# Performance work log

Hardware: AMD Instinct MI355X
Metric: run time of the kernel (lower is better)

The kernel has to match this reference:

```python
import jax, jax.numpy as jnp
import numpy as np

B, L, C, H, V = 64, 512, 256, 4, 32000
D = C // H
DIL = (1, 2, 4)
WIN = 3
NC = (50, 20)
NEG = -1e9


def setup_inputs() -> dict:
    key = jax.random.key(0)
    ks = jax.random.split(key, 20)
    g = lambda i, shape: jax.random.normal(ks[i], shape, jnp.float32) * 0.05
    Lay = len(DIL)
    x = jax.random.randint(ks[0], (B, L), 0, V)
    emb = g(1, (V, C)).at[0].set(0.0)  # padding_idx=0 row is zero
    return dict(
        x=x, emb=emb, pos=g(2, (L, C)),
        gp_W=g(3, (Lay, C, C)), gp_as=g(4, (Lay, H, D)), gp_ad=g(5, (Lay, H, D)),
        gf_W=g(6, (Lay, C, C)), gf_as=g(7, (Lay, H, D)), gf_ad=g(8, (Lay, H, D)),
        msg_W=g(9, (Lay, C, 2 * C)), msg_b=jnp.zeros((Lay, C), jnp.float32),
        gru_Wih=g(10, (Lay, 3 * C, C)), gru_bih=jnp.zeros((Lay, 3 * C), jnp.float32),
        gru_Whh=g(11, (Lay, 3 * C, C)), gru_bhh=jnp.zeros((Lay, 3 * C), jnp.float32),
        ln_g=jnp.ones((Lay, C), jnp.float32), ln_b=jnp.zeros((Lay, C), jnp.float32),
        pool_w=g(12, (C,)), pool_b=jnp.zeros((), jnp.float32),
        h0_W=g(13, (NC[0], C)), h0_b=jnp.zeros((NC[0],), jnp.float32),
        h1_W=g(14, (NC[1], C)), h1_b=jnp.zeros((NC[1],), jnp.float32),
    )


def _dense_gat(x, W, a_src, a_dst, adj):
    # x: [B,L,C], W: [C_out,C_in], a_*: [H,D], adj: [B,L,L] bool
    b, l, _ = x.shape
    h = jnp.einsum('blc,oc->blo', x, W).reshape(b, l, H, D).transpose(0, 2, 1, 3)  # [B,H,L,D]
    s = jnp.einsum('bhld,hd->bhl', h, a_src)
    d = jnp.einsum('bhld,hd->bhl', h, a_dst)
    e = s[:, :, :, None] + d[:, :, None, :]            # [B,H,L,L]
    e = jnp.where(e > 0, e, 0.2 * e)                   # LeakyReLU(0.2)
    e = jnp.where(adj[:, None, :, :], e, NEG)
    alpha = jax.nn.softmax(e, axis=-1)                 # dropout is identity in eval
    out = jnp.einsum('bhij,bhjd->bhid', alpha, h)
    return out.transpose(0, 2, 1, 3).reshape(b, l, C)


def _forward(x, emb, pos, gp_W, gp_as, gp_ad, gf_W, gf_as, gf_ad,
             msg_W, msg_b, gru_Wih, gru_bih, gru_Whh, gru_bhh,
             ln_g, ln_b, pool_w, pool_b, h0_W, h0_b, h1_W, h1_b):
    mask = x != 0                                      # [B,L]
    mf = mask.astype(jnp.float32)[..., None]           # [B,L,1]
    h = (emb[x] + pos[None, :, :] * mf) * mf
    logical = jnp.clip(jnp.cumsum(mask.astype(jnp.int32), axis=1) - 1, 0)
    valid = mask[:, None, :] & mask[:, :, None]        # [B,L,L]
    eye = jnp.eye(L, dtype=bool)[None]
    for l in range(len(DIL)):
        dil = DIL[l]
        diff = logical[:, :, None] - logical[:, None, :]
        ad = jnp.abs(diff)
        in_win = (ad <= WIN * dil) & (ad % dil == 0)
        adj_p = (valid & in_win & (diff < 0)) | eye
        adj_f = (valid & in_win & (diff > 0)) | eye
        m_p = _dense_gat(h, gp_W[l], gp_as[l], gp_ad[l], adj_p)
        m_f = _dense_gat(h, gf_W[l], gf_as[l], gf_ad[l], adj_f)
        m = jnp.concatenate([m_p, m_f], axis=-1)
        m = jax.nn.relu(jnp.einsum('blk,ck->blc', m, msg_W[l]) + msg_b[l])
        # GRUCell(input=m, hidden=h), PyTorch gate order: r,z,n
        gi = jnp.einsum('blc,gc->blg', m, gru_Wih[l]) + gru_bih[l]
        gh = jnp.einsum('blc,gc->blg', h, gru_Whh[l]) + gru_bhh[l]
        ir, iz, inn = jnp.split(gi, 3, axis=-1)
        hr, hz, hn = jnp.split(gh, 3, axis=-1)
        r = jax.nn.sigmoid(ir + hr)
        z = jax.nn.sigmoid(iz + hz)
        n = jnp.tanh(inn + r * hn)
        h_new = (1.0 - z) * n + z * h
        mu = jnp.mean(h_new, axis=-1, keepdims=True)
        var = jnp.mean(jnp.square(h_new - mu), axis=-1, keepdims=True)
        h_new = (h_new - mu) * jax.lax.rsqrt(var + 1e-5) * ln_g[l] + ln_b[l]
        h = h_new * mf
    # attention pooling over sequence (masked softmax on linear scores)
    sc = jnp.einsum('blc,c->bl', h, pool_w) + pool_b
    sc = jnp.where(mask, sc, NEG)
    a = jax.nn.softmax(sc, axis=-1)
    pooled = jnp.einsum('bl,blc->bc', a, h)            # dropout identity in eval
    o0 = pooled @ h0_W.T + h0_b
    o1 = pooled @ h1_W.T + h1_b
    return jnp.concatenate([o0, o1], axis=-1)          # [B, 50+20]


def reference(x, emb, pos, gp_W, gp_as, gp_ad, gf_W, gf_as, gf_ad,
              msg_W, msg_b, gru_Wih, gru_bih, gru_Whh, gru_bhh,
              ln_g, ln_b, pool_w, pool_b, h0_W, h0_b, h1_W, h1_b):
    return _forward(x, emb, pos, gp_W, gp_as, gp_ad, gf_W, gf_as, gf_ad,
                    msg_W, msg_b, gru_Wih, gru_bih, gru_Whh, gru_bhh,
                    ln_g, ln_b, pool_w, pool_b, h0_W, h0_b, h1_W, h1_b)
```

## Files before the change

kernel.cpp:

```cpp
#include <hip/hip_runtime.h>
#include <math.h>

#define B_ 64
#define L_ 512
#define C_ 256
#define H_ 4
#define LAY 3
#define NEGV -1e9f

typedef __attribute__((ext_vector_type(8))) short short8;
typedef __attribute__((ext_vector_type(4))) short short4v;
typedef __attribute__((ext_vector_type(4))) float floatx4;

static __device__ __forceinline__ float rcp_(float x) { return __builtin_amdgcn_rcpf(x); }
static __device__ __forceinline__ float sig_(float x) { return rcp_(1.f + __expf(-x)); }
static __device__ __forceinline__ float tanh_(float x) {
    float e = __expf(2.f * x);
    return 1.f - 2.f * rcp_(e + 1.f);
}

static __device__ __forceinline__ short f2bf(float f) {
    unsigned x = __float_as_uint(f);
    x += 0x7fffu + ((x >> 16) & 1u);
    return (short)(x >> 16);
}
static __device__ __forceinline__ float bf2f(short s) {
    return __uint_as_float(((unsigned)(unsigned short)s) << 16);
}

static __device__ __forceinline__ int tok_swizzle(int blk) {
    int c8 = blk & 7, i = blk >> 3;
    return (c8 + 8 * (i >> 5)) * 128 + (i & 31) * 4;
}

static __device__ __forceinline__ void gl_lds16(const short* g, short* l) {
    __builtin_amdgcn_global_load_lds(
        (const __attribute__((address_space(1))) unsigned int*)g,
        (__attribute__((address_space(3))) unsigned int*)l, 16, 0, 0);
}

#define CF() asm volatile("" ::: "memory")

#define PR_N0 (3 * 640 * 256)
#define PR_N1 (3 * 256 * 512)
#define PR_N2 (3 * 1024 * 512)
#define PR_N3 (3 * 1024)
#define PR_N4 (B_ * 70)
#define PR_TOT (PR_N0 + PR_N1 + PR_N2 + PR_N3 + PR_N4)

__global__ void prep_all(const float* __restrict__ gpW, const float* __restrict__ gfW,
                         const float* __restrict__ gpas, const float* __restrict__ gpad,
                         const float* __restrict__ gfas, const float* __restrict__ gfad,
                         const float* __restrict__ msgW,
                         const float* __restrict__ Wih, const float* __restrict__ Whh,
                         const float* __restrict__ bih, const float* __restrict__ bhh,
                         short* __restrict__ Wc, short* __restrict__ msgWb,
                         short* __restrict__ Bc, float* __restrict__ bias4,
                         float* __restrict__ outz) {
    int i = blockIdx.x * 256 + threadIdx.x;
    if (i < PR_N0) {
        int k = i & 255;
        int r = (i >> 8) % 640;
        int l = i / (640 * 256);
        float v = 0.f;
        if (r < 256) {
            v = gpW[((size_t)l * 256 + r) * 256 + k];
        } else if (r < 512) {
            v = gfW[((size_t)l * 256 + (r - 256)) * 256 + k];
        } else {
            int n = r - 512;
            if (n < 16) {
                int type = n >> 3, dir = (n >> 2) & 1, hh = n & 3;
                const float* a = type ? (dir ? gfad : gpad) : (dir ? gfas : gpas);
                const float* W = dir ? gfW : gpW;
                for (int j = 0; j < 64; j++) {
                    float av = a[l * 256 + hh * 64 + j];
                    float wv = W[((size_t)l * 256 + hh * 64 + j) * 256 + k];
                    v = fmaf(av, wv, v);
                }
            }
        }
        Wc[i] = f2bf(v);
        return;
    }
    i -= PR_N0;
    if (i < PR_N1) { msgWb[i] = f2bf(msgW[i]); return; }
    i -= PR_N1;
    if (i < PR_N2) {
        int k = i & 511, np = (i >> 9) & 1023, l = i >> 19;
        int ch = np >> 2, g = np & 3;
        float v = 0.f;
        if (g < 2) {
            v = (k < 256) ? Wih[((size_t)l * 768 + g * 256 + ch) * 256 + k]
                          : Whh[((size_t)l * 768 + g * 256 + ch) * 256 + (k - 256)];
        } else if (g == 2) {
            if (k < 256) v = Wih[((size_t)l * 768 + 512 + ch) * 256 + k];
        } else {
            if (k >= 256) v = Whh[((size_t)l * 768 + 512 + ch) * 256 + (k - 256)];
        }
        Bc[i] = f2bf(v);
        return;
    }
    i -= PR_N2;
    if (i < PR_N3) {
        int np = i & 1023, l = i >> 10;
        int ch = np >> 2, g = np & 3;
        float v;
        if (g < 2)       v = bih[l * 768 + g * 256 + ch] + bhh[l * 768 + g * 256 + ch];
        else if (g == 2) v = bih[l * 768 + 512 + ch];
        else             v = bhh[l * 768 + 512 + ch];
        bias4[i] = v;
        return;
    }
    i -= PR_N3;
    if (i < PR_N4) outz[i] = 0.f;
}

__global__ __launch_bounds__(512) void scan_embed(
    const int* __restrict__ x, const float* __restrict__ emb,
    const float* __restrict__ pos, short* __restrict__ hb,
    int* __restrict__ mask, int* __restrict__ logical,
    int* __restrict__ pol, int* __restrict__ nvalid) {
    if (blockIdx.x < 64) {
        int b = blockIdx.x, t = threadIdx.x;
        __shared__ int s[L_];
        int m = (x[b * L_ + t] != 0) ? 1 : 0;
        s[t] = m;
        __syncthreads();
        for (int off = 1; off < L_; off <<= 1) {
            int v = (t >= off) ? s[t - off] : 0;
            __syncthreads();
            s[t] += v;
            __syncthreads();
        }
        int cum = s[t];
        int lg = cum - 1; if (lg < 0) lg = 0;
        mask[b * L_ + t] = m;
        logical[b * L_ + t] = lg;
        if (m) pol[b * L_ + lg] = t;
        if (t == L_ - 1) nvalid[b] = cum;
    } else {
        int t = threadIdx.x & 255, sub = threadIdx.x >> 8;
        int blk2 = (blockIdx.x - 64) * 2 + sub;
        int bl = tok_swizzle(blk2) + (t >> 6);
        int lane = t & 63;
        int xv = x[bl];
        float mf = (xv != 0) ? 1.f : 0.f;
        int l = bl & (L_ - 1);
        float4 e = *(const float4*)&emb[(size_t)xv * C_ + lane * 4];
        float4 p = *(const float4*)&pos[(size_t)l * C_ + lane * 4];
        short4v hv4;
        hv4.x = f2bf((e.x + p.x * mf) * mf);
        hv4.y = f2bf((e.y + p.y * mf) * mf);
        hv4.z = f2bf((e.z + p.z * mf) * mf);
        hv4.w = f2bf((e.w + p.w * mf) * mf);
        *(short4v*)&hb[(size_t)bl * C_ + lane * 4] = hv4;
    }
}

static __device__ __forceinline__ short8 lds_rd8(const short* p) {
    return *(const short8*)p;
}

template <int MH>
static __device__ __forceinline__ void ld_af(const short* bufA, int wm, int q, int t16,
                                             short8 af[4][2]) {
#pragma unroll
    for (int mfl = 0; mfl < 4; ++mfl) {
        int row = wm * 128 + (MH * 4 + mfl) * 16 + t16;
#pragma unroll
        for (int ks = 0; ks < 2; ++ks) {
            int cg = (ks * 4 + q) ^ (row & 7);
            af[mfl][ks] = lds_rd8(&bufA[row * 64 + cg * 8]);
        }
    }
}

template <int NH>
static __device__ __forceinline__ void ld_bf(const short* bufB, int wn, int q, int t16,
                                             short8 bf[2][2]) {
#pragma unroll
    for (int nfl = 0; nfl < 2; ++nfl) {
        int row = wn * 64 + (NH * 2 + nfl) * 16 + t16;
#pragma unroll
        for (int ks = 0; ks < 2; ++ks) {
            int cg = (ks * 4 + q) ^ (row & 7);
            bf[nfl][ks] = lds_rd8(&bufB[row * 64 + cg * 8]);
        }
    }
}

static __device__ __forceinline__ void ld_bf32(const short* bufB, int wn, int q, int t16,
                                               short8 bf[2][2]) {
#pragma unroll
    for (int nfl = 0; nfl < 2; ++nfl) {
        int row = wn * 32 + nfl * 16 + t16;
#pragma unroll
        for (int ks = 0; ks < 2; ++ks) {
            int cg = (ks * 4 + q) ^ (row & 7);
            bf[nfl][ks] = lds_rd8(&bufB[row * 64 + cg * 8]);
        }
    }
}

template <int MH, int NH>
static __device__ __forceinline__ void mfma_q(const short8 af[4][2], const short8 bf[2][2],
                                              floatx4 acc[4][8]) {
    __builtin_amdgcn_s_setprio(1);
#pragma unroll
    for (int ks = 0; ks < 2; ++ks)
#pragma unroll
        for (int mfl = 0; mfl < 4; ++mfl)
#pragma unroll
            for (int nfl = 0; nfl < 2; ++nfl)
                acc[NH * 2 + nfl][MH * 4 + mfl] = __builtin_amdgcn_mfma_f32_16x16x32_bf16(
                    bf[nfl][ks], af[mfl][ks], acc[NH * 2 + nfl][MH * 4 + mfl], 0, 0, 0);
    __builtin_amdgcn_s_setprio(0);
}

template <int MH>
static __device__ __forceinline__ void mfma_m(const short8 af[4][2], const short8 bf[2][2],
                                              floatx4 acc[2][8]) {
    __builtin_amdgcn_s_setprio(1);
#pragma unroll
    for (int ks = 0; ks < 2; ++ks)
#pragma unroll
        for (int mfl = 0; mfl < 4; ++mfl)
#pragma unroll
            for (int nfl = 0; nfl < 2; ++nfl)
                acc[nfl][MH * 4 + mfl] = __builtin_amdgcn_mfma_f32_16x16x32_bf16(
                    bf[nfl][ks], af[mfl][ks], acc[nfl][MH * 4 + mfl], 0, 0, 0);
    __builtin_amdgcn_s_setprio(0);
}

__global__ __launch_bounds__(512, 2) void projssd_deep(const short* __restrict__ A0,
                                                       const short* __restrict__ Bw,
                                                       short* __restrict__ hpb2,
                                                       float* __restrict__ Ssd) {
    __shared__ short lds[2][24576];
    const int id = blockIdx.x;
    const int j = id >> 3;
    const int cb = j >> 4;
    const int rb = (id & 7) * 16 + (j & 15);
    const int tid = threadIdx.x;
    const int wave = tid >> 6, lane = tid & 63;
    const int wm = wave >> 2, wn = wave & 3;
    const int q = lane >> 4, t16 = lane & 15;
    const size_t arow0 = (size_t)rb * 256;
    const short* Bb = Bw + (size_t)cb * 128 * 256;

    floatx4 acc[2][8];
#pragma unroll
    for (int i = 0; i < 2; i++)
#pragma unroll
        for (int jj = 0; jj < 8; jj++) acc[i][jj] = (floatx4)0.f;

    auto stageA = [&](int t, int Hh) {
        short* bufA = lds[t & 1];
#pragma unroll
        for (int u = 0; u < 2; ++u) {
            int unit = u * 512 + tid;
            int row = Hh * 128 + (unit >> 3);
            int cs = (unit & 7) ^ (row & 7);
            gl_lds16(A0 + (arow0 + (size_t)row) * 256 + t * 64 + cs * 8,
                     bufA + Hh * 8192 + unit * 8);
        }
    };
    auto stageB = [&](int t) {
        short* bufB = lds[t & 1] + 16384;
#pragma unroll
        for (int u = 0; u < 2; ++u) {
            int unit = u * 512 + tid;
            int row = unit >> 3;
            int cs = (unit & 7) ^ (row & 7);
            gl_lds16(Bb + (size_t)row * 256 + t * 64 + cs * 8, bufB + unit * 8);
        }
    };

    stageA(0, 0); stageA(0, 1); stageB(0); stageB(1);
    asm volatile("s_waitcnt vmcnt(2)" ::: "memory");
    CF(); __builtin_amdgcn_s_barrier(); CF();

    short8 af[4][2], bfr[2][2];

#pragma unroll
    for (int t = 0; t < 4; ++t) {
        const short* bufA = lds[t & 1];
        const short* bufB = lds[t & 1] + 16384;

        ld_af<0>(bufA, wm, q, t16, af);
        ld_bf32(bufB, wn, q, t16, bfr);
        if (t < 3) { stageA(t + 1, 0); stageA(t + 1, 1); }
        CF(); __builtin_amdgcn_s_barrier();
        asm volatile("s_waitcnt lgkmcnt(0)" ::: "memory");
        __builtin_amdgcn_sched_barrier(0);
        mfma_m<0>(af, bfr, acc);
        CF(); __builtin_amdgcn_s_barrier(); CF();

        ld_af<1>(bufA, wm, q, t16, af);
        if (t < 2) stageB(t + 2);
        CF(); __builtin_amdgcn_s_barrier();
        asm volatile("s_waitcnt lgkmcnt(0)" ::: "memory");
        __builtin_amdgcn_sched_barrier(0);
        mfma_m<1>(af, bfr, acc);
        if (t < 2)       asm volatile("s_waitcnt vmcnt(2)" ::: "memory");
        else if (t == 2) asm volatile("s_waitcnt vmcnt(0)" ::: "memory");
        CF(); __builtin_amdgcn_s_barrier(); CF();
    }

    if (cb < 4) {
        short* sO = (short*)lds;
#pragma unroll
        for (int nf = 0; nf < 2; nf++) {
            int chl = wn * 32 + nf * 16 + q * 4;
#pragma unroll
            for (int mf = 0; mf < 8; mf++) {
                int rowl = wm * 128 + mf * 16 + t16;
                short4v pk;
                pk.x = f2bf(acc[nf][mf][0]);
                pk.y = f2bf(acc[nf][mf][1]);
                pk.z = f2bf(acc[nf][mf][2]);
                pk.w = f2bf(acc[nf][mf][3]);
                *(short4v*)&sO[rowl * 132 + chl] = pk;
            }
        }
        __syncthreads();
#pragma unroll
        for (int it = 0; it < 8; ++it) {
            int unit = it * 512 + tid;
            int rowl = unit >> 4, ck = unit & 15;
            *(short8*)&hpb2[(arow0 + rowl) * 512 + cb * 128 + ck * 8] =
                *(const short8*)&sO[rowl * 132 + ck * 8];
        }
    } else {
        if (wn == 0) {
            int chl = q * 4;
            if (chl < 16) {
#pragma unroll
                for (int mf = 0; mf < 8; mf++) {
                    int rowl = wm * 128 + mf * 16 + t16;
                    float4 pk = make_float4(acc[0][mf][0], acc[0][mf][1],
                                            acc[0][mf][2], acc[0][mf][3]);
                    *(float4*)&Ssd[(arow0 + rowl) * 16 + chl] = pk;
                }
            }
        }
    }
}

__global__ __launch_bounds__(512, 2) void gru_bgemm(const short* __restrict__ mmb,
                                                    const short* __restrict__ hb_in,
                                                    const short* __restrict__ Bw,
                                                    short* __restrict__ hn2b,
                                                    const float* __restrict__ bias4) {
    __shared__ short lds[2][32768];
    const int id = blockIdx.x;
    const int rb = 16 * (id & 7) + (id >> 5);
    const int cb = (id >> 3) & 3;
    const int tid = threadIdx.x;
    const int wave = tid >> 6, lane = tid & 63;
    const int wm = wave >> 2, wn = wave & 3;
    const int q = lane >> 4, t16 = lane & 15;
    const size_t arow0 = (size_t)rb * 256;
    const short* Bb = Bw + (size_t)cb * 256 * 512;
    const int ord0 = (5 + cb) & 7;

    floatx4 acc[4][8];
#pragma unroll
    for (int i = 0; i < 4; i++)
#pragma unroll
        for (int jj = 0; jj < 8; jj++) acc[i][jj] = (floatx4)0.f;

    auto stageA = [&](int i, int Hh) {
        int tt = (ord0 + i) & 7;
        const short* Asrc = (tt < 4) ? (mmb + tt * 64) : (hb_in + (tt - 4) * 64);
        short* bufA = lds[i & 1];
#pragma unroll
        for (int u = 0; u < 2; ++u) {
            int unit = u * 512 + tid;
            int row = Hh * 128 + (unit >> 3);
            int cs = (unit & 7) ^ (row & 7);
            gl_lds16(Asrc + (arow0 + (size_t)row) * 256 + cs * 8,
                     bufA + Hh * 8192 + unit * 8);
        }
    };
    auto stageB = [&](int i, int Hh) {
        int tt = (ord0 + i) & 7;
        short* bufB = lds[i & 1] + 16384;
#pragma unroll
        for (int u = 0; u < 2; ++u) {
            int unit = u * 512 + tid;
            int row = Hh * 128 + (unit >> 3);
            int cs = (unit & 7) ^ (row & 7);
            gl_lds16(Bb + (size_t)row * 512 + tt * 64 + cs * 8,
                     bufB + Hh * 8192 + unit * 8);
        }
    };

    stageA(0, 0); stageA(0, 1); stageB(0, 0); stageB(0, 1);
    stageA(1, 0); stageA(1, 1); stageB(1, 0); stageB(1, 1);
    asm volatile("s_waitcnt vmcnt(8)" ::: "memory");
    CF(); __builtin_amdgcn_s_barrier(); CF();

    short8 af[4][2], b0[2][2], b1[2][2];

#pragma unroll
    for (int t = 0; t < 8; ++t) {
        const short* bufA = lds[t & 1];
        const short* bufB = lds[t & 1] + 16384;

        ld_af<0>(bufA, wm, q, t16, af);
        ld_bf<0>(bufB, wn, q, t16, b0);
        CF(); __builtin_amdgcn_s_barrier();
        asm volatile("s_waitcnt lgkmcnt(0)" ::: "memory");
        __builtin_amdgcn_sched_barrier(0);
        mfma_q<0, 0>(af, b0, acc);
        CF(); __builtin_amdgcn_s_barrier(); CF();

        ld_bf<1>(bufB, wn, q, t16, b1);
        CF(); __builtin_amdgcn_s_barrier();
        asm volatile("s_waitcnt lgkmcnt(0)" ::: "memory");
        __builtin_amdgcn_sched_barrier(0);
        mfma_q<0, 1>(af, b1, acc);
        CF(); __builtin_amdgcn_s_barrier(); CF();

        ld_af<1>(bufA, wm, q, t16, af);
        if (t < 6) { stageB(t + 2, 0); stageB(t + 2, 1); }
        CF(); __builtin_amdgcn_s_barrier();
        asm volatile("s_waitcnt lgkmcnt(0)" ::: "memory");
        __builtin_amdgcn_sched_barrier(0);
        mfma_q<1, 1>(af, b1, acc);
        CF(); __builtin_amdgcn_s_barrier(); CF();

        if (t < 6) { stageA(t + 2, 0); stageA(t + 2, 1); }
        CF(); __builtin_amdgcn_s_barrier();
        mfma_q<1, 0>(af, b0, acc);
        if (t < 6)       asm volatile("s_waitcnt vmcnt(8)" ::: "memory");
        else if (t == 6) asm volatile("s_waitcnt vmcnt(0)" ::: "memory");
        CF(); __builtin_amdgcn_s_barrier(); CF();
    }

    const short* hpt = lds[1];
    short* sO = (short*)lds;
#pragma unroll
    for (int nf = 0; nf < 4; nf++) {
        int chl = wn * 16 + nf * 4 + q;
        int col0 = cb * 256 + wn * 64 + nf * 16 + q * 4;
        float4 bv4 = *(const float4*)&bias4[col0];
#pragma unroll
        for (int mf = 0; mf < 8; mf++) {
            int rowl = wm * 128 + mf * 16 + t16;
            float hp = bf2f(hpt[rowl * 64 + (((chl >> 3) ^ (rowl & 7)) << 3) + (chl & 7)]);
            float r = sig_(acc[nf][mf][0] + bv4.x);
            float z = sig_(acc[nf][mf][1] + bv4.y);
            float nv = tanh_((acc[nf][mf][2] + bv4.z) + r * (acc[nf][mf][3] + bv4.w));
            sO[rowl * 72 + chl] = f2bf((1.f - z) * nv + z * hp);
        }
    }
    __syncthreads();
#pragma unroll
    for (int it = 0; it < 4; ++it) {
        int unit = it * 512 + tid;
        int rowl = unit >> 3, ck = unit & 7;
        *(short8*)&hn2b[(arow0 + rowl) * 256 + cb * 64 + ck * 8] =
            *(const short8*)&sO[rowl * 72 + ck * 8];
    }
}

__global__ __launch_bounds__(512, 2) void msg_bgemm(const short* __restrict__ A0,
                                                    const short* __restrict__ Bw,
                                                    short* __restrict__ Cout,
                                                    const float* __restrict__ bias) {
    __shared__ short lds[2][24576];
    const int id = blockIdx.x;
    const int j = id >> 3;
    const int rb = (id & 7) * 16 + (j & 15);
    const int cb = j >> 4;
    const int tid = threadIdx.x;
    const int wave = tid >> 6, lane = tid & 63;
    const int wm = wave >> 2, wn = wave & 3;
    const int q = lane >> 4, t16 = lane & 15;
    const size_t arow0 = (size_t)rb * 256;
    const short* Bb = Bw + (size_t)cb * 128 * 512;

    floatx4 acc[2][8];
#pragma unroll
    for (int i = 0; i < 2; i++)
#pragma unroll
        for (int jj = 0; jj < 8; jj++) acc[i][jj] = (floatx4)0.f;

    auto stageA = [&](int t, int Hh) {
        short* bufA = lds[t & 1];
#pragma unroll
        for (int u = 0; u < 2; ++u) {
            int unit = u * 512 + tid;
            int row = Hh * 128 + (unit >> 3);
            int cs = (unit & 7) ^ (row & 7);
            gl_lds16(A0 + (arow0 + (size_t)row) * 512 + t * 64 + cs * 8,
                     bufA + Hh * 8192 + unit * 8);
        }
    };
    auto stageB = [&](int t) {
        short* bufB = lds[t & 1] + 16384;
#pragma unroll
        for (int u = 0; u < 2; ++u) {
            int unit = u * 512 + tid;
            int row = unit >> 3;
            int cs = (unit & 7) ^ (row & 7);
            gl_lds16(Bb + (size_t)row * 512 + t * 64 + cs * 8, bufB + unit * 8);
        }
    };

    stageA(0, 0); stageA(0, 1); stageB(0); stageB(1);
    asm volatile("s_waitcnt vmcnt(2)" ::: "memory");
    CF(); __builtin_amdgcn_s_barrier(); CF();

    short8 af[4][2], bfr[2][2];

#pragma unroll 2
    for (int t = 0; t < 8; ++t) {
        const short* bufA = lds[t & 1];
        const short* bufB = lds[t & 1] + 16384;

        ld_af<0>(bufA, wm, q, t16, af);
        ld_bf32(bufB, wn, q, t16, bfr);
        if (t < 7) { stageA(t + 1, 0); stageA(t + 1, 1); }
        CF(); __builtin_amdgcn_s_barrier();
        asm volatile("s_waitcnt lgkmcnt(0)" ::: "memory");
        mfma_m<0>(af, bfr, acc);
        CF(); __builtin_amdgcn_s_barrier(); CF();

        ld_af<1>(bufA, wm, q, t16, af);
        if (t < 6) stageB(t + 2);
        CF(); __builtin_amdgcn_s_barrier();
        asm volatile("s_waitcnt lgkmcnt(0)" ::: "memory");
        mfma_m<1>(af, bfr, acc);
        if (t < 6)       asm volatile("s_waitcnt vmcnt(2)" ::: "memory");
        else if (t == 6) asm volatile("s_waitcnt vmcnt(0)" ::: "memory");
        CF(); __builtin_amdgcn_s_barrier(); CF();
    }

    short* sO = (short*)lds;
#pragma unroll
    for (int nf = 0; nf < 2; nf++) {
        int chl = wn * 32 + nf * 16 + q * 4;
        int col0 = cb * 128 + chl;
        float4 bv4 = *(const float4*)&bias[col0];
#pragma unroll
        for (int mf = 0; mf < 8; mf++) {
            int rowl = wm * 128 + mf * 16 + t16;
            short4v pk;
            pk.x = f2bf(fmaxf(acc[nf][mf][0] + bv4.x, 0.f));
            pk.y = f2bf(fmaxf(acc[nf][mf][1] + bv4.y, 0.f));
            pk.z = f2bf(fmaxf(acc[nf][mf][2] + bv4.z, 0.f));
            pk.w = f2bf(fmaxf(acc[nf][mf][3] + bv4.w, 0.f));
            *(short4v*)&sO[rowl * 132 + chl] = pk;
        }
    }
    __syncthreads();
#pragma unroll
    for (int it = 0; it < 8; ++it) {
        int unit = it * 512 + tid;
        int rowl = unit >> 4, ck = unit & 15;
        *(short8*)&Cout[(arow0 + rowl) * 256 + cb * 128 + ck * 8] =
            *(const short8*)&sO[rowl * 132 + ck * 8];
    }
}

__global__ __launch_bounds__(256) void ln_kernel(
    const short* __restrict__ hn2b, short* __restrict__ hb,
    const int* __restrict__ mask,
    const float* __restrict__ lng, const float* __restrict__ lnb) {
    int t = threadIdx.x;
    int bl = tok_swizzle(blockIdx.x) + (t >> 6);
    int lane = t & 63;
    short4v v4 = *(const short4v*)&hn2b[(size_t)bl * C_ + lane * 4];
    float v[4] = {bf2f(v4.x), bf2f(v4.y), bf2f(v4.z), bf2f(v4.w)};
    float s = (v[0] + v[1]) + (v[2] + v[3]);
    float ss = (v[0] * v[0] + v[1] * v[1]) + (v[2] * v[2] + v[3] * v[3]);
#pragma unroll
    for (int off = 32; off; off >>= 1) {
        s += __shfl_xor(s, off);
        ss += __shfl_xor(ss, off);
    }
    float mu = s * (1.f / 256.f);
    float var = ss * (1.f / 256.f) - mu * mu;
    float rstd = rsqrtf(fmaxf(var, 0.f) + 1e-5f);
    float4 lg = *(const float4*)&lng[lane * 4];
    float4 lb = *(const float4*)&lnb[lane * 4];
    float mfv = mask[bl] ? 1.f : 0.f;
    short4v yb;
    yb.x = f2bf(((v[0] - mu) * rstd * lg.x + lb.x) * mfv);
    yb.y = f2bf(((v[1] - mu) * rstd * lg.y + lb.y) * mfv);
    yb.z = f2bf(((v[2] - mu) * rstd * lg.z + lb.z) * mfv);
    yb.w = f2bf(((v[3] - mu) * rstd * lg.w + lb.w) * mfv);
    *(short4v*)&hb[(size_t)bl * C_ + lane * 4] = yb;
}

__global__ __launch_bounds__(256) void agg_fused(
    const short* __restrict__ hpb2, const float* __restrict__ S,
    const int* __restrict__ mask, const int* __restrict__ logical,
    const int* __restrict__ pol, const int* __restrict__ nvalid,
    short* __restrict__ m, int dil) {
    int t = threadIdx.x;
    int bl = tok_swizzle(blockIdx.x) + (t >> 6);
    int sub = t & 63;
    int dir = sub >> 5;
    int slot = sub & 31;
    int cb = slot * 8;
    int head = slot >> 3;
    int b = bl >> 9;

    int mi = mask[bl];
    int li = logical[bl];
    int nv = nvalid[b];
    int js[3]; int nn = 0;
    if (mi) {
#pragma unroll
        for (int k = 1; k <= 3; k++) {
            int lj = dir ? (li - k * dil) : (li + k * dil);
            if (lj >= 0 && lj < nv) js[nn++] = pol[b * L_ + lj];
        }
    }
    int sn = dir * 4 + head, dn = 8 + sn;
    float si = S[(size_t)bl * 16 + sn];
    float di = S[(size_t)bl * 16 + dn];
    float e0 = si + di; e0 = e0 > 0.f ? e0 : 0.2f * e0;
    float emax = e0, ev[3];
    for (int k = 0; k < nn; k++) {
        float djv = S[((size_t)(b * L_ + js[k])) * 16 + dn];
        float e = si + djv; e = e > 0.f ? e : 0.2f * e;
        ev[k] = e; emax = fmaxf(emax, e);
    }
    float w0 = __expf(e0 - emax), den = w0;
    float wv[3];
    for (int k = 0; k < nn; k++) { wv[k] = __expf(ev[k] - emax); den += wv[k]; }
    float rden = rcp_(den);

    size_t base = (size_t)bl * 512 + dir * 256 + cb;
    short8 vself = *(const short8*)&hpb2[base];
    float o[8];
#pragma unroll
    for (int j = 0; j < 8; j++) o[j] = w0 * bf2f(vself[j]);
    for (int k = 0; k < nn; k++) {
        short8 vn = *(const short8*)&hpb2[((size_t)(b * L_ + js[k])) * 512 + dir * 256 + cb];
#pragma unroll
        for (int j = 0; j < 8; j++) o[j] = fmaf(wv[k], bf2f(vn[j]), o[j]);
    }
    short8 ov;
#pragma unroll
    for (int j = 0; j < 8; j++) ov[j] = f2bf(o[j] * rden);
    *(short8*)&m[base] = ov;
}

__global__ __launch_bounds__(1024) void pool_head2(
    const short* __restrict__ hb, const int* __restrict__ mask,
    const float* __restrict__ pw, const float* __restrict__ pb,
    const float* __restrict__ h0W, const float* __restrict__ h0b,
    const float* __restrict__ h1W, const float* __restrict__ h1b,
    float* __restrict__ out) {
    int b = blockIdx.x >> 2, s = blockIdx.x & 3;
    int t = threadIdx.x;
    int lane = t & 63, wave = t >> 6;
    __shared__ float sc[L_];
    __shared__ float red[20];
    __shared__ float part[16][64];
    __shared__ float pooled[64];

    float4 wv = *(const float4*)&pw[lane * 4];
    for (int l = wave; l < L_; l += 16) {
        short4v hv = *(const short4v*)&hb[((size_t)b * L_ + l) * C_ + lane * 4];
        float p = bf2f(hv.x) * wv.x + bf2f(hv.y) * wv.y
                + bf2f(hv.z) * wv.z + bf2f(hv.w) * wv.w;
#pragma unroll
        for (int off = 32; off; off >>= 1) p += __shfl_down(p, off);
        if (lane == 0) sc[l] = mask[b * L_ + l] ? (p + pb[0]) : NEGV;
    }
    __syncthreads();

    float v = (t < L_) ? sc[t] : NEGV;
    float mx = v;
#pragma unroll
    for (int off = 32; off; off >>= 1) mx = fmaxf(mx, __shfl_down(mx, off));
    if (lane == 0) red[wave] = mx;
    __syncthreads();
    if (t == 0) {
        float g = red[0];
        for (int i = 1; i < 16; i++) g = fmaxf(g, red[i]);
        red[16] = g;
    }
    __syncthreads();
    float gmax = red[16];
    float e = (t < L_) ? __expf(v - gmax) : 0.f;
    float ssum = e;
#pragma unroll
    for (int off = 32; off; off >>= 1) ssum += __shfl_down(ssum, off);
    if (lane == 0) red[wave] = ssum;
    __syncthreads();
    if (t == 0) {
        float g = 0.f;
        for (int i = 0; i < 16; i++) g += red[i];
        red[17] = 1.f / g;
    }
    __syncthreads();
    if (t < L_) sc[t] = e * red[17];
    __syncthreads();

    {
        int c0 = t & 63, lw = t >> 6;
        const short* hcol = &hb[((size_t)b * L_ + lw * 32) * C_ + s * 64 + c0];
        const float* scg = &sc[lw * 32];
        float a0 = 0.f, a1 = 0.f;
        for (int l = 0; l < 32; l += 2) {
            a0 = fmaf(scg[l + 0], bf2f(hcol[(size_t)(l + 0) * C_]), a0);
            a1 = fmaf(scg[l + 1], bf2f(hcol[(size_t)(l + 1) * C_]), a1);
        }
        part[lw][c0] = a0 + a1;
    }
    __syncthreads();
    if (t < 64) {
        float p = 0.f;
        for (int i = 0; i < 16; i++) p += part[i][t];
        pooled[t] = p;
    }
    __syncthreads();

    for (int o = wave; o < 70; o += 16) {
        const float* W = (o < 50) ? (h0W + (size_t)o * C_) : (h1W + (size_t)(o - 50) * C_);
        float sv = pooled[lane] * W[s * 64 + lane];
#pragma unroll
        for (int off = 32; off; off >>= 1) sv += __shfl_down(sv, off);
        if (lane == 0) {
            float add = sv + ((s == 0) ? ((o < 50) ? h0b[o] : h1b[o - 50]) : 0.f);
            atomicAdd(&out[b * 70 + o], add);
        }
    }
}

extern "C" void kernel_launch(void* const* d_in, const int* in_sizes, int n_in,
                              void* d_out, int out_size, void* d_ws, size_t ws_size,
                              hipStream_t stream) {
    const int*   x    = (const int*)d_in[0];
    const float* emb  = (const float*)d_in[1];
    const float* pos  = (const float*)d_in[2];
    const float* gpW  = (const float*)d_in[3];
    const float* gpas = (const float*)d_in[4];
    const float* gpad = (const float*)d_in[5];
    const float* gfW  = (const float*)d_in[6];
    const float* gfas = (const float*)d_in[7];
    const float* gfad = (const float*)d_in[8];
    const float* msgW = (const float*)d_in[9];
    const float* msgb = (const float*)d_in[10];
    const float* Wih  = (const float*)d_in[11];
    const float* bih  = (const float*)d_in[12];
    const float* Whh  = (const float*)d_in[13];
    const float* bhh  = (const float*)d_in[14];
    const float* lng  = (const float*)d_in[15];
    const float* lnb  = (const float*)d_in[16];
    const float* pw   = (const float*)d_in[17];
    const float* pb   = (const float*)d_in[18];
    const float* h0W  = (const float*)d_in[19];
    const float* h0b  = (const float*)d_in[20];
    const float* h1W  = (const float*)d_in[21];
    const float* h1b  = (const float*)d_in[22];
    float* out = (float*)d_out;

    const size_t MW = 1024 * 1024;
    float* ws = (float*)d_ws;
    short* hn2b = (short*)ws;
    short* hb   = (short*)(ws + 8 * MW);
    short* mmb  = (short*)(ws + 12 * MW);
    float* Ssd  = ws + 12 * MW;
    short* hpb2 = (short*)(ws + 16 * MW);
    short* mb   = (short*)(ws + 24 * MW);
    short* Wcomb = (short*)(ws + 32 * MW);
    short* msgWb = Wcomb + 3 * 640 * 256;
    short* Bcat  = msgWb + 3 * 256 * 512;
    float* bias4 = (float*)(Bcat + 3 * 1024 * 512);
    int* mask    = (int*)(bias4 + 3 * 1024);
    int* logical = mask + B_ * L_;
    int* pol     = logical + B_ * L_;
    int* nvalid  = pol + B_ * L_;

    prep_all<<<(PR_TOT + 255) / 256, 256, 0, stream>>>(
        gpW, gfW, gpas, gpad, gfas, gfad, msgW, Wih, Whh, bih, bhh,
        Wcomb, msgWb, Bcat, bias4, out);

    scan_embed<<<64 + 4096, 512, 0, stream>>>(x, emb, pos, hb, mask, logical, pol, nvalid);

    const int DILS[LAY] = {1, 2, 4};

    for (int l = 0; l < LAY; l++) {
        int dil = DILS[l];
        projssd_deep<<<640, 512, 0, stream>>>(hb, Wcomb + (size_t)l * 640 * 256,
                                              hpb2, Ssd);
        agg_fused<<<8192, 256, 0, stream>>>(hpb2, Ssd, mask, logical, pol, nvalid, mb, dil);
        msg_bgemm<<<256, 512, 0, stream>>>(mb, msgWb + (size_t)l * 256 * 512,
                                           mmb, msgb + l * C_);
        gru_bgemm<<<512, 512, 0, stream>>>(mmb, hb, Bcat + (size_t)l * 1024 * 512,
                                           hn2b, bias4 + l * 1024);
        ln_kernel<<<8192, 256, 0, stream>>>(hn2b, hb, mask, lng + l * C_, lnb + l * C_);
    }

    pool_head2<<<B_ * 4, 1024, 0, stream>>>(hb, mask, pw, pb, h0W, h0b, h1W, h1b, out);
}
```

Measured before the change: 483.4 us.

## Restructure GRU GEMM to 32-wide K tiles with triple-buffered A

The GRU batched GEMM now walks K in 16 steps of 32 instead of 8 steps of 64. A uses a three-slot LDS ring and B a two-slot ring, which shrinks LDS from 128 KB to 80 KB. Launch bounds are raised to allow four blocks per SM, aiming for more occupancy and finer-grained load/compute overlap. The trade-off is twice as many barriers and waitcnt stalls per K, and a more intricate buffer mapping for reading the previous hidden state in the epilogue.

```diff
diff --git a/kernel.cpp b/kernel.cpp
--- a/kernel.cpp
+++ b/kernel.cpp
@@ -176,46 +176,17 @@
     }
 }
 
-template <int NH>
-static __device__ __forceinline__ void ld_bf(const short* bufB, int wn, int q, int t16,
-                                             short8 bf[2][2]) {
+static __device__ __forceinline__ void ld_bf32(const short* bufB, int wn, int q, int t16,
+                                               short8 bf[2][2]) {
 #pragma unroll
     for (int nfl = 0; nfl < 2; ++nfl) {
-        int row = wn * 64 + (NH * 2 + nfl) * 16 + t16;
+        int row = wn * 32 + nfl * 16 + t16;
 #pragma unroll
         for (int ks = 0; ks < 2; ++ks) {
             int cg = (ks * 4 + q) ^ (row & 7);
             bf[nfl][ks] = lds_rd8(&bufB[row * 64 + cg * 8]);
         }
     }
-}
-
-static __device__ __forceinline__ void ld_bf32(const short* bufB, int wn, int q, int t16,
-                                               short8 bf[2][2]) {
-#pragma unroll
-    for (int nfl = 0; nfl < 2; ++nfl) {
-        int row = wn * 32 + nfl * 16 + t16;
-#pragma unroll
-        for (int ks = 0; ks < 2; ++ks) {
-            int cg = (ks * 4 + q) ^ (row & 7);
-            bf[nfl][ks] = lds_rd8(&bufB[row * 64 + cg * 8]);
-        }
-    }
-}
-
-template <int MH, int NH>
-static __device__ __forceinline__ void mfma_q(const short8 af[4][2], const short8 bf[2][2],
-                                              floatx4 acc[4][8]) {
-    __builtin_amdgcn_s_setprio(1);
-#pragma unroll
-    for (int ks = 0; ks < 2; ++ks)
-#pragma unroll
-        for (int mfl = 0; mfl < 4; ++mfl)
-#pragma unroll
-            for (int nfl = 0; nfl < 2; ++nfl)
-                acc[NH * 2 + nfl][MH * 4 + mfl] = __builtin_amdgcn_mfma_f32_16x16x32_bf16(
-                    bf[nfl][ks], af[mfl][ks], acc[NH * 2 + nfl][MH * 4 + mfl], 0, 0, 0);
-    __builtin_amdgcn_s_setprio(0);
 }
 
 template <int MH>
@@ -230,6 +201,40 @@
             for (int nfl = 0; nfl < 2; ++nfl)
                 acc[nfl][MH * 4 + mfl] = __builtin_amdgcn_mfma_f32_16x16x32_bf16(
                     bf[nfl][ks], af[mfl][ks], acc[nfl][MH * 4 + mfl], 0, 0, 0);
+    __builtin_amdgcn_s_setprio(0);
+}
+
+template <int MH>
+static __device__ __forceinline__ void ld_af32(const short* bufA, int wm, int q, int t16,
+                                               short8 af[4]) {
+#pragma unroll
+    for (int mfl = 0; mfl < 4; ++mfl) {
+        int row = wm * 128 + (MH * 4 + mfl) * 16 + t16;
+        int cg = q ^ (row & 3);
+        af[mfl] = lds_rd8(&bufA[row * 32 + cg * 8]);
+    }
+}
+
+static __device__ __forceinline__ void ld_bfq(const short* bufB, int wn, int q, int t16,
+                                              short8 bf[4]) {
+#pragma unroll
+    for (int nf = 0; nf < 4; ++nf) {
+        int row = wn * 64 + nf * 16 + t16;
+        int cg = q ^ (row & 3);
+        bf[nf] = lds_rd8(&bufB[row * 32 + cg * 8]);
+    }
+}
+
+template <int MH>
+static __device__ __forceinline__ void mfma_h(const short8 af[4], const short8 bf[4],
+                                              floatx4 acc[4][8]) {
+    __builtin_amdgcn_s_setprio(1);
+#pragma unroll
+    for (int mfl = 0; mfl < 4; ++mfl)
+#pragma unroll
+        for (int nf = 0; nf < 4; ++nf)
+            acc[nf][MH * 4 + mfl] = __builtin_amdgcn_mfma_f32_16x16x32_bf16(
+                bf[nf], af[mfl], acc[nf][MH * 4 + mfl], 0, 0, 0);
     __builtin_amdgcn_s_setprio(0);
 }
 
@@ -348,12 +353,13 @@
     }
 }
 
-__global__ __launch_bounds__(512, 2) void gru_bgemm(const short* __restrict__ mmb,
+#define GA_OFF(k3) ((k3) == 0 ? 0 : ((k3) == 1 ? 16384 : 8192))
+__global__ __launch_bounds__(512, 4) void gru_bgemm(const short* __restrict__ mmb,
                                                     const short* __restrict__ hb_in,
                                                     const short* __restrict__ Bw,
                                                     short* __restrict__ hn2b,
                                                     const float* __restrict__ bias4) {
-    __shared__ short lds[2][32768];
+    __shared__ short lds[40960];
     const int id = blockIdx.x;
     const int rb = 16 * (id & 7) + (id >> 5);
     const int cb = (id >> 3) & 3;
@@ -363,7 +369,7 @@
     const int q = lane >> 4, t16 = lane & 15;
     const size_t arow0 = (size_t)rb * 256;
     const short* Bb = Bw + (size_t)cb * 256 * 512;
-    const int ord0 = (5 + cb) & 7;
+    const int ord0 = (2 * cb + 10) & 15;
 
     floatx4 acc[4][8];
 #pragma unroll
@@ -371,86 +377,75 @@
 #pragma unroll
         for (int jj = 0; jj < 8; jj++) acc[i][jj] = (floatx4)0.f;
 
-    auto stageA = [&](int i, int Hh) {
-        int tt = (ord0 + i) & 7;
-        const short* Asrc = (tt < 4) ? (mmb + tt * 64) : (hb_in + (tt - 4) * 64);
-        short* bufA = lds[i & 1];
+    auto stageA = [&](int i) {
+        int tt = (ord0 + i) & 15;
+        const short* Asrc = (tt < 8) ? (mmb + tt * 32) : (hb_in + (tt - 8) * 32);
+        short* bufA = lds + GA_OFF(i % 3);
 #pragma unroll
         for (int u = 0; u < 2; ++u) {
             int unit = u * 512 + tid;
-            int row = Hh * 128 + (unit >> 3);
-            int cs = (unit & 7) ^ (row & 7);
-            gl_lds16(Asrc + (arow0 + (size_t)row) * 256 + cs * 8,
-                     bufA + Hh * 8192 + unit * 8);
+            int row = unit >> 2;
+            int cs = (unit & 3) ^ (row & 3);
+            gl_lds16(Asrc + (arow0 + (size_t)row) * 256 + cs * 8, bufA + unit * 8);
         }
     };
-    auto stageB = [&](int i, int Hh) {
-        int tt = (ord0 + i) & 7;
-        short* bufB = lds[i & 1] + 16384;
+    auto stageB = [&](int i) {
+        int tt = (ord0 + i) & 15;
+        short* bufB = lds + 24576 + (i & 1) * 8192;
 #pragma unroll
         for (int u = 0; u < 2; ++u) {
             int unit = u * 512 + tid;
-            int row = Hh * 128 + (unit >> 3);
-            int cs = (unit & 7) ^ (row & 7);
-            gl_lds16(Bb + (size_t)row * 512 + tt * 64 + cs * 8,
-                     bufB + Hh * 8192 + unit * 8);
+            int row = unit >> 2;
+            int cs = (unit & 3) ^ (row & 3);
+            gl_lds16(Bb + (size_t)row * 512 + tt * 32 + cs * 8, bufB + unit * 8);
         }
     };
 
-    stageA(0, 0); stageA(0, 1); stageB(0, 0); stageB(0, 1);
-    stageA(1, 0); stageA(1, 1); stageB(1, 0); stageB(1, 1);
-    asm volatile("s_waitcnt vmcnt(8)" ::: "memory");
+    stageA(0); stageB(0); stageA(1); stageB(1);
+    asm volatile("s_waitcnt vmcnt(4)" ::: "memory");
     CF(); __builtin_amdgcn_s_barrier(); CF();
 
-    short8 af[4][2], b0[2][2], b1[2][2];
-
-#pragma unroll
-    for (int t = 0; t < 8; ++t) {
-        const short* bufA = lds[t & 1];
-        const short* bufB = lds[t & 1] + 16384;
-
-        ld_af<0>(bufA, wm, q, t16, af);
-        ld_bf<0>(bufB, wn, q, t16, b0);
+    short8 af[4], bf[4];
+
+#pragma unroll
+    for (int t = 0; t < 16; ++t) {
+        const short* bufA = lds + GA_OFF(t % 3);
+        const short* bufB = lds + 24576 + (t & 1) * 8192;
+
+        ld_af32<0>(bufA, wm, q, t16, af);
+        ld_bfq(bufB, wn, q, t16, bf);
+        if (t < 14) stageA(t + 2);
         CF(); __builtin_amdgcn_s_barrier();
         asm volatile("s_waitcnt lgkmcnt(0)" ::: "memory");
         __builtin_amdgcn_sched_barrier(0);
-        mfma_q<0, 0>(af, b0, acc);
+        mfma_h<0>(af, bf, acc);
         CF(); __builtin_amdgcn_s_barrier(); CF();
 
-        ld_bf<1>(bufB, wn, q, t16, b1);
+        ld_af32<1>(bufA, wm, q, t16, af);
+        if (t < 14) stageB(t + 2);
         CF(); __builtin_amdgcn_s_barrier();
         asm volatile("s_waitcnt lgkmcnt(0)" ::: "memory");
         __builtin_amdgcn_sched_barrier(0);
-        mfma_q<0, 1>(af, b1, acc);
+        mfma_h<1>(af, bf, acc);
+        if (t < 14)       asm volatile("s_waitcnt vmcnt(4)" ::: "memory");
+        else if (t == 14) asm volatile("s_waitcnt vmcnt(0)" ::: "memory");
         CF(); __builtin_amdgcn_s_barrier(); CF();
-
-        ld_af<1>(bufA, wm, q, t16, af);
-        if (t < 6) { stageB(t + 2, 0); stageB(t + 2, 1); }
-        CF(); __builtin_amdgcn_s_barrier();
-        asm volatile("s_waitcnt lgkmcnt(0)" ::: "memory");
-        __builtin_amdgcn_sched_barrier(0);
-        mfma_q<1, 1>(af, b1, acc);
-        CF(); __builtin_amdgcn_s_barrier(); CF();
-
-        if (t < 6) { stageA(t + 2, 0); stageA(t + 2, 1); }
-        CF(); __builtin_amdgcn_s_barrier();
-        mfma_q<1, 0>(af, b0, acc);
-        if (t < 6)       asm volatile("s_waitcnt vmcnt(8)" ::: "memory");
-        else if (t == 6) asm volatile("s_waitcnt vmcnt(0)" ::: "memory");
-        CF(); __builtin_amdgcn_s_barrier(); CF();
-    }
-
-    const short* hpt = lds[1];
-    short* sO = (short*)lds;
+    }
+
+    const short* hpLo = lds + 8192;
+    const short* hpHi = lds;
+    short* sO = lds + 16384;
 #pragma unroll
     for (int nf = 0; nf < 4; nf++) {
         int chl = wn * 16 + nf * 4 + q;
         int col0 = cb * 256 + wn * 64 + nf * 16 + q * 4;
         float4 bv4 = *(const float4*)&bias4[col0];
+        const short* hpt = (chl >> 5) ? hpHi : hpLo;
+        int c32 = chl & 31;
 #pragma unroll
         for (int mf = 0; mf < 8; mf++) {
             int rowl = wm * 128 + mf * 16 + t16;
-            float hp = bf2f(hpt[rowl * 64 + (((chl >> 3) ^ (rowl & 7)) << 3) + (chl & 7)]);
+            float hp = bf2f(hpt[rowl * 32 + (((c32 >> 3) ^ (rowl & 3)) << 3) + (c32 & 7)]);
             float r = sig_(acc[nf][mf][0] + bv4.x);
             float z = sig_(acc[nf][mf][1] + bv4.y);
             float nv = tanh_((acc[nf][mf][2] + bv4.z) + r * (acc[nf][mf][3] + bv4.w));
```

New measurement: 1.552 ms. 221% more time.

## Fold final-layer LayerNorm into attention pooling head algebraically

Applied to the files above, without the earlier changes.

Skips the last layer's standalone LayerNorm kernel and computes per-row mean and rstd inside the pooling kernel, reading the pre-LN GRU output directly. Pooling scores and the pooled vector are recovered algebraically through gamma/beta-folded weights and a mean correction term, so the normalized tensor is never materialized. This removes one full-tensor read/write pass and a kernel launch. In exchange it computes variance as E[x^2]-mu^2 from bf16 inputs, which may differ slightly in precision, and the pooling kernel does more reductions.

```diff
diff --git a/kernel.cpp b/kernel.cpp
--- a/kernel.cpp
+++ b/kernel.cpp
@@ -653,9 +653,10 @@
     *(short8*)&m[base] = ov;
 }
 
-__global__ __launch_bounds__(1024) void pool_head2(
-    const short* __restrict__ hb, const int* __restrict__ mask,
+__global__ __launch_bounds__(1024) void pool_head_ln(
+    const short* __restrict__ hn2b, const int* __restrict__ mask,
     const float* __restrict__ pw, const float* __restrict__ pb,
+    const float* __restrict__ lng2, const float* __restrict__ lnb2,
     const float* __restrict__ h0W, const float* __restrict__ h0b,
     const float* __restrict__ h1W, const float* __restrict__ h1b,
     float* __restrict__ out) {
@@ -663,18 +664,46 @@
     int t = threadIdx.x;
     int lane = t & 63, wave = t >> 6;
     __shared__ float sc[L_];
-    __shared__ float red[20];
+    __shared__ float muA[L_];
+    __shared__ float rsA[L_];
+    __shared__ float red[24];
     __shared__ float part[16][64];
     __shared__ float pooled[64];
 
     float4 wv = *(const float4*)&pw[lane * 4];
+    float4 gv = *(const float4*)&lng2[lane * 4];
+    float4 bv = *(const float4*)&lnb2[lane * 4];
+    float pg0 = wv.x * gv.x, pg1 = wv.y * gv.y, pg2 = wv.z * gv.z, pg3 = wv.w * gv.w;
+    float cG = (pg0 + pg1) + (pg2 + pg3);
+    float cB = (wv.x * bv.x + wv.y * bv.y) + (wv.z * bv.z + wv.w * bv.w);
+#pragma unroll
+    for (int off = 32; off; off >>= 1) {
+        cG += __shfl_xor(cG, off);
+        cB += __shfl_xor(cB, off);
+    }
+    float pb0 = pb[0];
+
     for (int l = wave; l < L_; l += 16) {
-        short4v hv = *(const short4v*)&hb[((size_t)b * L_ + l) * C_ + lane * 4];
-        float p = bf2f(hv.x) * wv.x + bf2f(hv.y) * wv.y
-                + bf2f(hv.z) * wv.z + bf2f(hv.w) * wv.w;
-#pragma unroll
-        for (int off = 32; off; off >>= 1) p += __shfl_down(p, off);
-        if (lane == 0) sc[l] = mask[b * L_ + l] ? (p + pb[0]) : NEGV;
+        short4v hv = *(const short4v*)&hn2b[((size_t)b * L_ + l) * C_ + lane * 4];
+        float h0 = bf2f(hv.x), h1 = bf2f(hv.y), h2 = bf2f(hv.z), h3 = bf2f(hv.w);
+        float s1 = pg0 * h0 + pg1 * h1 + pg2 * h2 + pg3 * h3;
+        float s2 = (h0 + h1) + (h2 + h3);
+        float s3 = (h0 * h0 + h1 * h1) + (h2 * h2 + h3 * h3);
+#pragma unroll
+        for (int off = 32; off; off >>= 1) {
+            s1 += __shfl_down(s1, off);
+            s2 += __shfl_down(s2, off);
+            s3 += __shfl_down(s3, off);
+        }
+        if (lane == 0) {
+            float mu = s2 * (1.f / 256.f);
+            float var = s3 * (1.f / 256.f) - mu * mu;
+            float rstd = rsqrtf(fmaxf(var, 0.f) + 1e-5f);
+            int mk = mask[b * L_ + l];
+            sc[l] = mk ? (rstd * (s1 - mu * cG) + cB + pb0) : NEGV;
+            muA[l] = mu;
+            rsA[l] = mk ? rstd : 0.f;
+        }
     }
     __syncthreads();
 
@@ -703,12 +732,24 @@
         red[17] = 1.f / g;
     }
     __syncthreads();
-    if (t < L_) sc[t] = e * red[17];
+    float a = e * red[17];
+    float arv = (t < L_) ? a * rsA[t] : 0.f;
+    float amu = (t < L_) ? arv * muA[t] : 0.f;
+    if (t < L_) sc[t] = arv;
+#pragma unroll
+    for (int off = 32; off; off >>= 1) amu += __shfl_down(amu, off);
+    if (lane == 0) red[wave] = amu;
+    __syncthreads();
+    if (t == 0) {
+        float g = 0.f;
+        for (int i = 0; i < 16; i++) g += red[i];
+        red[18] = g;
+    }
     __syncthreads();
 
     {
         int c0 = t & 63, lw = t >> 6;
-        const short* hcol = &hb[((size_t)b * L_ + lw * 32) * C_ + s * 64 + c0];
+        const short* hcol = &hn2b[((size_t)b * L_ + lw * 32) * C_ + s * 64 + c0];
         const float* scg = &sc[lw * 32];
         float a0 = 0.f, a1 = 0.f;
         for (int l = 0; l < 32; l += 2) {
@@ -721,7 +762,8 @@
     if (t < 64) {
         float p = 0.f;
         for (int i = 0; i < 16; i++) p += part[i][t];
-        pooled[t] = p;
+        int c = s * 64 + t;
+        pooled[t] = lng2[c] * (p - red[18]) + lnb2[c];
     }
     __syncthreads();
 
@@ -799,8 +841,11 @@
                                            mmb, msgb + l * C_);
         gru_bgemm<<<512, 512, 0, stream>>>(mmb, hb, Bcat + (size_t)l * 1024 * 512,
                                            hn2b, bias4 + l * 1024);
-        ln_kernel<<<8192, 256, 0, stream>>>(hn2b, hb, mask, lng + l * C_, lnb + l * C_);
-    }
-
-    pool_head2<<<B_ * 4, 1024, 0, stream>>>(hb, mask, pw, pb, h0W, h0b, h1W, h1b, out);
-}
+        if (l < 2)
+            ln_kernel<<<8192, 256, 0, stream>>>(hn2b, hb, mask, lng + l * C_, lnb + l * C_);
+    }
+
+    pool_head_ln<<<B_ * 4, 1024, 0, stream>>>(hn2b, mask, pw, pb,
+                                              lng + 2 * C_, lnb + 2 * C_,
+                                              h0W, h0b, h1W, h1b, out);
+}
```

Result: no change. 480.7 us (-0.6%).
